# Kernel optimization log

Measured on AMD Instinct MI355X. Metric: run time of the kernel, lower is better.

Reference implementation:

```python
import jax, jax.numpy as jnp
import numpy as np

K = 5              # kernel_size per pseudo dim
K3 = K ** 3        # 125 kernel weight slots
BITS = np.array([[(c >> d) & 1 for d in range(3)] for c in range(8)], dtype=np.int32)  # [8,3]
STRIDES = np.array([1, K, K * K], dtype=np.int32)

N0, E0 = 16384, 262144
N1, E1 = 4096, 65536
N2, E2 = 1024, 16384
N3, E3 = 256, 4096
B = 16
V = B * 8          # final dense 2x2x2 voxels per graph


def spline_conv(x, src, dst, pseudo, W, root, bias, num_nodes):
    """Degree-1 open B-spline conv (torch SplineConv, mean aggr + root + bias).
    x: [N,in], pseudo: [E,3] in [0,1], W: [K^3,in,out]."""
    v = pseudo * (K - 1)                         # [E,3]
    lo = jnp.clip(jnp.floor(v), 0, K - 2)
    frac = v - lo                                # [E,3]
    lo = lo.astype(jnp.int32)
    bits = jnp.asarray(BITS)                     # [8,3]
    idx = lo[:, None, :] + bits[None]            # [E,8,3]
    kidx = (idx * jnp.asarray(STRIDES)).sum(-1)  # [E,8] flat kernel index
    basis = jnp.where(bits[None].astype(bool), frac[:, None, :], 1.0 - frac[:, None, :]).prod(-1)  # [E,8]
    y = jnp.einsum('ni,kio->nko', x, W)          # [N,K3,out] per-node per-kernel transform
    yv = y[src[:, None], kidx]                   # [E,8,out] gather
    msg = (basis[..., None] * yv).sum(1)         # [E,out]
    agg = jax.ops.segment_sum(msg, dst, num_segments=num_nodes)
    deg = jax.ops.segment_sum(jnp.ones(dst.shape[0], x.dtype), dst, num_segments=num_nodes)
    agg = agg / jnp.maximum(deg, 1.0)[:, None]   # mean aggregation
    return agg + x @ root + bias


def pool_max(x, cluster, num_segments):
    p = jax.ops.segment_max(x, cluster, num_segments=num_segments)
    return jnp.where(jnp.isfinite(p), p, 0.0)    # empty voxels -> 0


def setup_inputs() -> dict:
    key = jax.random.key(0)
    ks = iter(jax.random.split(key, 64))
    f = lambda s, sc: jax.random.normal(next(ks), s, jnp.float32) * sc
    u = lambda s: jax.random.uniform(next(ks), s, jnp.float32)
    ri = lambda s, hi: jax.random.randint(next(ks), s, 0, hi, dtype=jnp.int32)
    return dict(
        x0=u((N0, 1)),
        pseudo0=u((E0, 3)), pseudo1=u((E1, 3)), pseudo2=u((E2, 3)), pseudo3=u((E3, 3)),
        W1=f((K3, 1, 32), 0.3), root1=f((1, 32), 0.3), b1=f((32,), 0.05),
        W2=f((K3, 32, 64), 0.05), root2=f((32, 64), 0.05), b2=f((64,), 0.05),
        W3=f((K3, 64, 64), 0.04), root3=f((64, 64), 0.04), b3=f((64,), 0.05),
        W4=f((K3, 64, 128), 0.04), root4=f((64, 128), 0.04), b4=f((128,), 0.05),
        fc1_w=f((1024, 256), 0.03), fc1_b=f((256,), 0.05),
        fc2_w=f((256, 10), 0.06), fc2_b=f((10,), 0.05),
        src0=ri((E0,), N0), dst0=ri((E0,), N0),
        src1=ri((E1,), N1), dst1=ri((E1,), N1),
        src2=ri((E2,), N2), dst2=ri((E2,), N2),
        src3=ri((E3,), N3), dst3=ri((E3,), N3),
        cluster0=ri((N0,), N1), cluster1=ri((N1,), N2),
        cluster2=ri((N2,), N3), cluster3=ri((N3,), V),
    )


def reference(x0, pseudo0, pseudo1, pseudo2, pseudo3,
              W1, root1, b1, W2, root2, b2, W3, root3, b3, W4, root4, b4,
              fc1_w, fc1_b, fc2_w, fc2_b,
              src0, dst0, src1, dst1, src2, dst2, src3, dst3,
              cluster0, cluster1, cluster2, cluster3):
    x = jax.nn.elu(spline_conv(x0, src0, dst0, pseudo0, W1, root1, b1, N0))
    x = pool_max(x, cluster0, N1)
    x = jax.nn.elu(spline_conv(x, src1, dst1, pseudo1, W2, root2, b2, N1))
    x = pool_max(x, cluster1, N2)
    x = jax.nn.elu(spline_conv(x, src2, dst2, pseudo2, W3, root3, b3, N2))
    x = pool_max(x, cluster2, N3)
    x = jax.nn.elu(spline_conv(x, src3, dst3, pseudo3, W4, root4, b4, N3))
    x = pool_max(x, cluster3, V)                 # [B*8, 128]
    x = x.reshape(B, 8 * 128)
    x = jax.nn.elu(x @ fc1_w + fc1_b)
    x = x @ fc2_w + fc2_b                        # dropout is a no-op in eval
    return jax.nn.log_softmax(x, axis=1)
```

## Files before the change

### kernel.cpp

```cpp
#include <hip/hip_runtime.h>
#include <hip/hip_bf16.h>
#include <math.h>

namespace {

typedef unsigned long long u64;
typedef __attribute__((ext_vector_type(8))) short bf16x8;
typedef __attribute__((ext_vector_type(4))) float f32x4;
typedef __attribute__((ext_vector_type(4))) unsigned uint4e;

constexpr int KK = 5;
constexpr int K3 = 125;
constexpr int N0 = 16384, E0 = 262144;
constexpr int N1 = 4096,  E1 = 65536;
constexpr int N2 = 1024,  E2 = 16384;
constexpr int N3 = 256,   E3 = 4096;
constexpr int E_TOT = E0 + E1 + E2 + E3;
constexpr unsigned ENC_NEG_INF = 0x007FFFFFu;
constexpr int KO2 = K3 * 64, KO3 = K3 * 64, KO4 = K3 * 128;

constexpr size_t A_PENC1 = 0;
constexpr size_t A_PENC2 = A_PENC1 + (size_t)N1 * 32;
constexpr size_t A_PENC3 = A_PENC2 + (size_t)N2 * 64;
constexpr size_t A_PENC4 = A_PENC3 + (size_t)N3 * 64;
constexpr size_t A_PENC_END = A_PENC4 + (size_t)128 * 128;
constexpr size_t PENC_TOTAL = A_PENC_END;

constexpr size_t A_WT2 = A_PENC_END;
constexpr size_t A_WT3 = A_WT2 + (size_t)K3 * 64 * 32 / 2;
constexpr size_t A_WT4 = A_WT3 + (size_t)K3 * 64 * 64 / 2;

constexpr size_t A_OFF0 = A_WT4 + (size_t)K3 * 128 * 64 / 2;
constexpr size_t A_OFF1 = A_OFF0 + (N0 + 4);
constexpr size_t A_OFF2 = A_OFF1 + (N1 + 4);
constexpr size_t A_OFF3 = A_OFF2 + (N2 + 4);
constexpr size_t A_CUR0 = A_OFF3 + (N3 + 4);
constexpr size_t A_CUR1 = A_CUR0 + N0;
constexpr size_t A_CUR2 = A_CUR1 + N1;
constexpr size_t A_CUR3 = A_CUR2 + N2;
constexpr size_t A_CUR_END = A_CUR3 + N3;
constexpr size_t CUR_TOTAL = A_CUR_END - A_CUR0;

constexpr size_t A_REC0 = (A_CUR_END + 3) & ~(size_t)3;
constexpr size_t A_REC1 = A_REC0 + (size_t)E0 * 12;
constexpr size_t A_REC2 = A_REC1 + (size_t)E1 * 12;
constexpr size_t A_REC3 = A_REC2 + (size_t)E2 * 12;
constexpr size_t A_Y    = (A_REC3 + (size_t)E3 * 12 + 3) & ~(size_t)3;

constexpr int NB_HIST  = (E_TOT + 255) / 256;
constexpr int NB_SCAT0 = E0 / 256;
constexpr int NB_SCAT1 = E1 / 256;
constexpr int NB_SCAT2 = E2 / 256;
constexpr int NB_SCAT3 = E3 / 256;
constexpr int NB_L1    = N0 / 8;
constexpr int NB_G2    = (KO2 / 64) * ((N1 / 16) / 16);
constexpr int NB_G3    = (KO3 / 64) * ((N2 / 16) / 16);
constexpr int NB_G4    = (KO4 / 64) * ((N3 / 16) / 16);
constexpr int NB_GA2   = N1 / 4;
constexpr int NB_GA3   = N2 / 4;
constexpr int NB_GA4   = N3 / 4;

struct __align__(16) ERec {
    float4 q0;
    float4 q1;
    u64 kid;
    unsigned src;
    unsigned pad;
};

struct P {
    const float *x0, *W1, *root1, *b1, *root2, *b2, *root3, *b3, *root4, *b4;
    const float *ps0, *ps1, *ps2, *ps3;
    const float *W2, *W3, *W4, *fc1w, *fc1b, *fc2w, *fc2b;
    const int *src0, *dst0, *src1, *dst1, *src2, *dst2, *src3, *dst3;
    const int *cl0, *cl1, *cl2, *cl3;
    float* ws;
    float* out;
};

__device__ __forceinline__ float eluf(float x) { return x > 0.f ? x : expm1f(x); }

__device__ __forceinline__ unsigned enc_f(float x) {
    unsigned u = __float_as_uint(x);
    return (u & 0x80000000u) ? ~u : (u | 0x80000000u);
}
__device__ __forceinline__ float dec_fin(unsigned u) {
    u = (u & 0x80000000u) ? (u & 0x7fffffffu) : ~u;
    float v = __uint_as_float(u);
    return isfinite(v) ? v : 0.f;
}
__device__ __forceinline__ float bf2f(unsigned short u) {
    return __uint_as_float((unsigned)u << 16);
}
__device__ __forceinline__ unsigned short f2bf(float v) {
    __hip_bfloat16 h = __float2bfloat16(v);
    return *reinterpret_cast<unsigned short*>(&h);
}

__device__ __forceinline__ ERec nt_load_rec(const ERec* p) {
    const uint4e* q = (const uint4e*)p;
    uint4e a = __builtin_nontemporal_load(q);
    uint4e b = __builtin_nontemporal_load(q + 1);
    uint4e c = __builtin_nontemporal_load(q + 2);
    ERec r;
    r.q0 = make_float4(__uint_as_float(a[0]), __uint_as_float(a[1]),
                       __uint_as_float(a[2]), __uint_as_float(a[3]));
    r.q1 = make_float4(__uint_as_float(b[0]), __uint_as_float(b[1]),
                       __uint_as_float(b[2]), __uint_as_float(b[3]));
    r.kid = (u64)c[0] | ((u64)c[1] << 32);
    r.src = c[2];
    r.pad = c[3];
    return r;
}
__device__ __forceinline__ void nt_store_rec(ERec* p, const ERec& r) {
    uint4e a = {__float_as_uint(r.q0.x), __float_as_uint(r.q0.y),
                __float_as_uint(r.q0.z), __float_as_uint(r.q0.w)};
    uint4e b = {__float_as_uint(r.q1.x), __float_as_uint(r.q1.y),
                __float_as_uint(r.q1.z), __float_as_uint(r.q1.w)};
    uint4e c = {(unsigned)(r.kid & 0xffffffffu), (unsigned)(r.kid >> 32), r.src, r.pad};
    uint4e* q = (uint4e*)p;
    __builtin_nontemporal_store(a, q);
    __builtin_nontemporal_store(b, q + 1);
    __builtin_nontemporal_store(c, q + 2);
}
__device__ __forceinline__ unsigned short nt_lds(const unsigned short* p) {
    return __builtin_nontemporal_load(p);
}

__device__ __forceinline__ void decode_edge(const float* __restrict__ pseudo, int e,
                                            float bas[8], int kid[8]) {
    float v0 = pseudo[e * 3 + 0] * (KK - 1);
    float v1 = pseudo[e * 3 + 1] * (KK - 1);
    float v2 = pseudo[e * 3 + 2] * (KK - 1);
    float f0 = fminf(fmaxf(floorf(v0), 0.f), (float)(KK - 2));
    float f1 = fminf(fmaxf(floorf(v1), 0.f), (float)(KK - 2));
    float f2 = fminf(fmaxf(floorf(v2), 0.f), (float)(KK - 2));
    int lo0 = (int)f0, lo1 = (int)f1, lo2 = (int)f2;
    float fr0 = v0 - f0, fr1 = v1 - f1, fr2 = v2 - f2;
#pragma unroll
    for (int c = 0; c < 8; ++c) {
        int b0 = c & 1, b1 = (c >> 1) & 1, b2 = (c >> 2) & 1;
        kid[c] = (lo0 + b0) + (lo1 + b1) * KK + (lo2 + b2) * KK * KK;
        bas[c] = (b0 ? fr0 : 1.f - fr0) * (b1 ? fr1 : 1.f - fr1) * (b2 ? fr2 : 1.f - fr2);
    }
}

__device__ void wt_unit(const float* __restrict__ W, unsigned short* __restrict__ wt,
                        int IN, int OUT, int k, float* smem) {
    const float* Wk = W + (size_t)k * IN * OUT;
    unsigned short* wk = wt + (size_t)k * IN * OUT;
    int halves = IN / 32;
    for (int h = 0; h < halves; ++h) {
        __syncthreads();
        for (int idx = threadIdx.x; idx < 32 * OUT; idx += 256) {
            int i = idx / OUT, o = idx % OUT;
            smem[i * (OUT + 1) + o] = Wk[(size_t)(h * 32 + i) * OUT + o];
        }
        __syncthreads();
        for (int idx = threadIdx.x; idx < OUT * 32; idx += 256) {
            int o = idx / 32, i = idx % 32;
            wk[(size_t)o * IN + h * 32 + i] = f2bf(smem[i * (OUT + 1) + o]);
        }
    }
}

__device__ void scat_unit(int u, const float* __restrict__ ps,
                          const int* __restrict__ dst, const int* __restrict__ srcA,
                          int* __restrict__ cur, ERec* __restrict__ rec, int E) {
    int e = u * 256 + threadIdx.x;
    if (e >= E) return;
    float b[8]; int k[8];
    decode_edge(ps, e, b, k);
    u64 pk = 0;
#pragma unroll
    for (int c = 0; c < 8; ++c) pk |= (u64)(unsigned)k[c] << (8 * c);
    int q = atomicAdd(&cur[dst[e]], 1);
    ERec r;
    r.q0 = make_float4(b[0], b[1], b[2], b[3]);
    r.q1 = make_float4(b[4], b[5], b[6], b[7]);
    r.kid = pk;
    r.src = (unsigned)srcA[e];
    r.pad = 0;
    nt_store_rec(&rec[q], r);
}

template <int IN>
__device__ __forceinline__ void gemm_tile(int n0, int ko0,
                                          const unsigned* __restrict__ penc,
                                          const unsigned short* __restrict__ wt,
                                          unsigned short* __restrict__ y, int KO) {
    int lane = threadIdx.x & 63;
    int l15 = lane & 15;
    int kk = (lane >> 4) << 3;
    int rbase = (lane >> 4) << 2;
    f32x4 acc[4];
#pragma unroll
    for (int t = 0; t < 4; ++t) acc[t] = (f32x4){0.f, 0.f, 0.f, 0.f};
#pragma unroll
    for (int s = 0; s < IN / 32; ++s) {
        const unsigned* pp = penc + (size_t)(n0 + l15) * IN + s * 32 + kk;
        uint4 u0 = *(const uint4*)pp;
        uint4 u1 = *(const uint4*)(pp + 4);
        unsigned uu[8] = {u0.x, u0.y, u0.z, u0.w, u1.x, u1.y, u1.z, u1.w};
        bf16x8 bfrag;
#pragma unroll
        for (int t = 0; t < 8; ++t) bfrag[t] = (short)f2bf(dec_fin(uu[t]));
#pragma unroll
        for (int t = 0; t < 4; ++t) {
            bf16x8 afrag = *(const bf16x8*)(wt + (size_t)(ko0 + t * 16 + l15) * IN + s * 32 + kk);
            acc[t] = __builtin_amdgcn_mfma_f32_16x16x32_bf16(afrag, bfrag, acc[t], 0, 0, 0);
        }
    }
#pragma unroll
    for (int t = 0; t < 4; ++t) {
        u64 pk = (u64)f2bf(acc[t][0]) | ((u64)f2bf(acc[t][1]) << 16)
               | ((u64)f2bf(acc[t][2]) << 32) | ((u64)f2bf(acc[t][3]) << 48);
        __builtin_nontemporal_store(pk, (u64*)(y + (size_t)(n0 + l15) * KO + ko0 + t * 16 + rbase));
    }
}

template <int IN>
__device__ void gemm_blk(int bid, const unsigned* __restrict__ penc,
                         const unsigned short* __restrict__ wt,
                         unsigned short* __restrict__ y, int N, int KO) {
    int nGrp = (N >> 4) >> 4;
    int kog = bid / nGrp;
    int nchunk = bid % nGrp;
    int wsub = threadIdx.x >> 6;
    int ko0 = kog << 6;
#pragma unroll
    for (int it = 0; it < 4; ++it) {
        int ntile = (nchunk << 4) + (it << 2) + wsub;
        gemm_tile<IN>(ntile << 4, ko0, penc, wt, y, KO);
    }
}

template <int IN, int OUT>
__device__ void gather_unit(int u, const unsigned short* __restrict__ y,
                            const ERec* __restrict__ rec, const int* __restrict__ off,
                            const unsigned* __restrict__ penc_prev,
                            const float* __restrict__ root,
                            const float* __restrict__ bias,
                            const int* __restrict__ cl,
                            unsigned* __restrict__ penc) {
    constexpr int KO = K3 * OUT;
    constexpr int WPT = OUT / 64;
    int lane = threadIdx.x & 63;
    int wv = threadIdx.x >> 6;
    int n = u * 4 + wv;
    int s0 = off[n], s1 = off[n + 1];
    float acc0 = 0.f, acc1 = 0.f;
    int j = s0;
    for (; j + 2 <= s1; j += 2) {
        ERec ra = nt_load_rec(&rec[j]), rb = nt_load_rec(&rec[j + 1]);
        const unsigned short* ypa = y + (size_t)ra.src * KO + lane;
        const unsigned short* ypb = y + (size_t)rb.src * KO + lane;
        float ba[8] = {ra.q0.x, ra.q0.y, ra.q0.z, ra.q0.w, ra.q1.x, ra.q1.y, ra.q1.z, ra.q1.w};
        float bb[8] = {rb.q0.x, rb.q0.y, rb.q0.z, rb.q0.w, rb.q1.x, rb.q1.y, rb.q1.z, rb.q1.w};
        u64 ka = ra.kid, kb = rb.kid;
        float va[8], vb[8], va2[8], vb2[8];
#pragma unroll
        for (int c = 0; c < 8; ++c) {
            int kca = (int)((ka >> (8 * c)) & 255u);
            int kcb = (int)((kb >> (8 * c)) & 255u);
            va[c] = bf2f(nt_lds(ypa + (size_t)kca * OUT));
            vb[c] = bf2f(nt_lds(ypb + (size_t)kcb * OUT));
            if (WPT == 2) {
                va2[c] = bf2f(nt_lds(ypa + (size_t)kca * OUT + 64));
                vb2[c] = bf2f(nt_lds(ypb + (size_t)kcb * OUT + 64));
            }
        }
#pragma unroll
        for (int c = 0; c < 8; ++c) {
            acc0 = fmaf(ba[c], va[c], acc0);
            acc0 = fmaf(bb[c], vb[c], acc0);
            if (WPT == 2) {
                acc1 = fmaf(ba[c], va2[c], acc1);
                acc1 = fmaf(bb[c], vb2[c], acc1);
            }
        }
    }
    if (j < s1) {
        ERec r = nt_load_rec(&rec[j]);
        const unsigned short* yp = y + (size_t)r.src * KO + lane;
        float b[8] = {r.q0.x, r.q0.y, r.q0.z, r.q0.w, r.q1.x, r.q1.y, r.q1.z, r.q1.w};
        u64 k8 = r.kid;
#pragma unroll
        for (int c = 0; c < 8; ++c) {
            int kc = (int)((k8 >> (8 * c)) & 255u);
            acc0 = fmaf(b[c], bf2f(nt_lds(yp + (size_t)kc * OUT)), acc0);
            if (WPT == 2) acc1 = fmaf(b[c], bf2f(nt_lds(yp + (size_t)kc * OUT + 64)), acc1);
        }
    }
    float dg = fmaxf((float)(s1 - s0), 1.f);
    float accs[2] = {acc0, acc1};
#pragma unroll
    for (int w = 0; w < WPT; ++w) {
        int o = lane + 64 * w;
        float r = 0.f;
        for (int i = 0; i < IN; ++i)
            r = fmaf(dec_fin(penc_prev[(size_t)n * IN + i]), root[(size_t)i * OUT + o], r);
        float val = accs[w] / dg + r + bias[o];
        val = eluf(val);
        atomicMax(&penc[(size_t)cl[n] * OUT + o], enc_f(val));
    }
}


__global__ __launch_bounds__(256) void k_p1(P p) {
    __shared__ float smem[32 * 129];
    float* ws = p.ws;
    int bid = blockIdx.x;
    if (bid < NB_HIST) {
        int g = bid * 256 + threadIdx.x;
        if (g < (int)PENC_TOTAL) ((unsigned*)(ws + A_PENC1))[g] = ENC_NEG_INF;
        if (g >= E_TOT) return;
        const int* dst; int* cur; int e;
        if (g < E0)                { dst = p.dst0; cur = (int*)(ws + A_CUR0); e = g; }
        else if (g < E0 + E1)      { dst = p.dst1; cur = (int*)(ws + A_CUR1); e = g - E0; }
        else if (g < E0 + E1 + E2) { dst = p.dst2; cur = (int*)(ws + A_CUR2); e = g - E0 - E1; }
        else                       { dst = p.dst3; cur = (int*)(ws + A_CUR3); e = g - E0 - E1 - E2; }
        atomicAdd(&cur[dst[e]], 1);
    } else {
        wt_unit(p.W2, (unsigned short*)(ws + A_WT2), 32, 64, bid - NB_HIST, smem);
    }
}

__global__ __launch_bounds__(1024) void k_scan(P p) {
    __shared__ int ls[1024];
    float* ws = p.ws;
    int* cur; int* off; int N;
    switch (blockIdx.x) {
        case 0:  cur = (int*)(ws + A_CUR0); off = (int*)(ws + A_OFF0); N = N0; break;
        case 1:  cur = (int*)(ws + A_CUR1); off = (int*)(ws + A_OFF1); N = N1; break;
        case 2:  cur = (int*)(ws + A_CUR2); off = (int*)(ws + A_OFF2); N = N2; break;
        default: cur = (int*)(ws + A_CUR3); off = (int*)(ws + A_OFF3); N = N3; break;
    }
    int t = threadIdx.x;
    int chunk = (N + 1023) >> 10;
    int b0 = t * chunk;
    int b1 = min(b0 + chunk, N);
    int s = 0;
    for (int i = b0; i < b1; ++i) s += cur[i];
    ls[t] = s;
    __syncthreads();
    for (int d = 1; d < 1024; d <<= 1) {
        int v = (t >= d) ? ls[t - d] : 0;
        __syncthreads();
        ls[t] += v;
        __syncthreads();
    }
    int run = (t == 0) ? 0 : ls[t - 1];
    for (int i = b0; i < b1; ++i) {
        int c = cur[i];
        off[i] = run;
        cur[i] = run;
        run += c;
    }
    if (t == 1023) off[N] = run;
}

__global__ __launch_bounds__(256) void k_p2(P p) {
    scat_unit(blockIdx.x, p.ps0, p.dst0, p.src0,
              (int*)(p.ws + A_CUR0), (ERec*)(p.ws + A_REC0), E0);
}

__global__ __launch_bounds__(256) void k_l1(P p) {
    __shared__ float wlds[K3 * 32];
    float* ws = p.ws;
    int bid = blockIdx.x;
    if (bid >= NB_L1) {
        scat_unit(bid - NB_L1, p.ps1, p.dst1, p.src1,
                  (int*)(ws + A_CUR1), (ERec*)(ws + A_REC1), E1);
        return;
    }
    for (int i = threadIdx.x; i < K3 * 32; i += 256) wlds[i] = p.W1[i];
    __syncthreads();
    const ERec* rec = (const ERec*)(ws + A_REC0);
    const int* off = (const int*)(ws + A_OFF0);
    unsigned* penc = (unsigned*)(ws + A_PENC1);
    int o = threadIdx.x & 31;
    int nsub = threadIdx.x >> 5;
    int n = bid * 8 + nsub;
    int s0 = off[n], s1 = off[n + 1];
    float acc = 0.f;
    int j = s0;
    for (; j + 2 <= s1; j += 2) {
        ERec ra = nt_load_rec(&rec[j]), rb = nt_load_rec(&rec[j + 1]);
        u64 ka = ra.kid, kb = rb.kid;
        float xa = p.x0[ra.src], xb = p.x0[rb.src];
        float ma, mb;
        ma  = ra.q0.x * wlds[((int)( ka        & 255u)) * 32 + o];
        ma += ra.q0.y * wlds[((int)((ka >>  8) & 255u)) * 32 + o];
        ma += ra.q0.z * wlds[((int)((ka >> 16) & 255u)) * 32 + o];
        ma += ra.q0.w * wlds[((int)((ka >> 24) & 255u)) * 32 + o];
        ma += ra.q1.x * wlds[((int)((ka >> 32) & 255u)) * 32 + o];
        ma += ra.q1.y * wlds[((int)((ka >> 40) & 255u)) * 32 + o];
        ma += ra.q1.z * wlds[((int)((ka >> 48) & 255u)) * 32 + o];
        ma += ra.q1.w * wlds[((int)((ka >> 56) & 255u)) * 32 + o];
        mb  = rb.q0.x * wlds[((int)( kb        & 255u)) * 32 + o];
        mb += rb.q0.y * wlds[((int)((kb >>  8) & 255u)) * 32 + o];
        mb += rb.q0.z * wlds[((int)((kb >> 16) & 255u)) * 32 + o];
        mb += rb.q0.w * wlds[((int)((kb >> 24) & 255u)) * 32 + o];
        mb += rb.q1.x * wlds[((int)((kb >> 32) & 255u)) * 32 + o];
        mb += rb.q1.y * wlds[((int)((kb >> 40) & 255u)) * 32 + o];
        mb += rb.q1.z * wlds[((int)((kb >> 48) & 255u)) * 32 + o];
        mb += rb.q1.w * wlds[((int)((kb >> 56) & 255u)) * 32 + o];
        acc = fmaf(xa, ma, fmaf(xb, mb, acc));
    }
    if (j < s1) {
        ERec r = nt_load_rec(&rec[j]);
        u64 k8 = r.kid;
        float xv = p.x0[r.src];
        float m;
        m  = r.q0.x * wlds[((int)( k8        & 255u)) * 32 + o];
        m += r.q0.y * wlds[((int)((k8 >>  8) & 255u)) * 32 + o];
        m += r.q0.z * wlds[((int)((k8 >> 16) & 255u)) * 32 + o];
        m += r.q0.w * wlds[((int)((k8 >> 24) & 255u)) * 32 + o];
        m += r.q1.x * wlds[((int)((k8 >> 32) & 255u)) * 32 + o];
        m += r.q1.y * wlds[((int)((k8 >> 40) & 255u)) * 32 + o];
        m += r.q1.z * wlds[((int)((k8 >> 48) & 255u)) * 32 + o];
        m += r.q1.w * wlds[((int)((k8 >> 56) & 255u)) * 32 + o];
        acc = fmaf(xv, m, acc);
    }
    float dg = fmaxf((float)(s1 - s0), 1.f);
    float val = acc / dg + p.x0[n] * p.root1[o] + p.b1[o];
    val = eluf(val);
    atomicMax(&penc[(size_t)p.cl0[n] * 32 + o], enc_f(val));
}

__global__ __launch_bounds__(256) void k_g2(P p) {
    __shared__ float smem[32 * 129];
    float* ws = p.ws;
    int bid = blockIdx.x;
    if (bid < NB_G2) {
        gemm_blk<32>(bid, (unsigned*)(ws + A_PENC1), (unsigned short*)(ws + A_WT2),
                     (unsigned short*)(ws + A_Y), N1, KO2);
    } else if (bid < NB_G2 + NB_SCAT2) {
        scat_unit(bid - NB_G2, p.ps2, p.dst2, p.src2,
                  (int*)(ws + A_CUR2), (ERec*)(ws + A_REC2), E2);
    } else if (bid < NB_G2 + NB_SCAT2 + K3) {
        wt_unit(p.W3, (unsigned short*)(ws + A_WT3), 64, 64, bid - NB_G2 - NB_SCAT2, smem);
    } else {
        wt_unit(p.W4, (unsigned short*)(ws + A_WT4), 64, 128, bid - NB_G2 - NB_SCAT2 - K3, smem);
    }
}

__global__ __launch_bounds__(256) void k_ga2(P p) {
    float* ws = p.ws;
    int bid = blockIdx.x;
    if (bid < NB_GA2) {
        gather_unit<32, 64>(bid, (unsigned short*)(ws + A_Y), (const ERec*)(ws + A_REC1),
                            (const int*)(ws + A_OFF1), (unsigned*)(ws + A_PENC1),
                            p.root2, p.b2, p.cl1, (unsigned*)(ws + A_PENC2));
    } else {
        scat_unit(bid - NB_GA2, p.ps3, p.dst3, p.src3,
                  (int*)(ws + A_CUR3), (ERec*)(ws + A_REC3), E3);
    }
}

__global__ __launch_bounds__(256) void k_g3(P p) {
    gemm_blk<64>(blockIdx.x, (unsigned*)(p.ws + A_PENC2), (unsigned short*)(p.ws + A_WT3),
                 (unsigned short*)(p.ws + A_Y), N2, KO3);
}
__global__ __launch_bounds__(256) void k_ga3(P p) {
    gather_unit<64, 64>(blockIdx.x, (unsigned short*)(p.ws + A_Y), (const ERec*)(p.ws + A_REC2),
                        (const int*)(p.ws + A_OFF2), (unsigned*)(p.ws + A_PENC2),
                        p.root3, p.b3, p.cl2, (unsigned*)(p.ws + A_PENC3));
}
__global__ __launch_bounds__(256) void k_g4(P p) {
    gemm_blk<64>(blockIdx.x, (unsigned*)(p.ws + A_PENC3), (unsigned short*)(p.ws + A_WT4),
                 (unsigned short*)(p.ws + A_Y), N3, KO4);
}
__global__ __launch_bounds__(256) void k_ga4(P p) {
    gather_unit<64, 128>(blockIdx.x, (unsigned short*)(p.ws + A_Y), (const ERec*)(p.ws + A_REC3),
                         (const int*)(p.ws + A_OFF3), (unsigned*)(p.ws + A_PENC3),
                         p.root4, p.b4, p.cl3, (unsigned*)(p.ws + A_PENC4));
}

__global__ __launch_bounds__(1024) void k_fc(P p) {
    __shared__ float xs[1024];
    __shared__ float part[4][257];
    __shared__ float h[256];
    __shared__ float l[10];
    __shared__ float red[2];
    int bq = blockIdx.x;
    int t = threadIdx.x;
    const unsigned* penc4 = (const unsigned*)(p.ws + A_PENC4);
    xs[t] = dec_fin(penc4[(size_t)bq * 1024 + t]);
    __syncthreads();
    int o = t & 255, sl = t >> 8;
    const float* wp = p.fc1w + (size_t)(sl * 256) * 256 + o;
    const float* xp = xs + sl * 256;
    float acc = 0.f;
#pragma unroll 8
    for (int k = 0; k < 256; ++k)
        acc = fmaf(xp[k], wp[(size_t)k * 256], acc);
    part[sl][o] = acc;
    __syncthreads();
    if (t < 256) {
        float v = part[0][t] + part[1][t] + part[2][t] + part[3][t] + p.fc1b[t];
        h[t] = eluf(v);
    }
    __syncthreads();
    if (t < 10) {
        float a2 = p.fc2b[t];
        for (int q = 0; q < 256; ++q)
            a2 = fmaf(h[q], p.fc2w[(size_t)q * 10 + t], a2);
        l[t] = a2;
    }
    __syncthreads();
    if (t == 0) {
        float m = l[0];
        for (int i = 1; i < 10; ++i) m = fmaxf(m, l[i]);
        float s = 0.f;
        for (int i = 0; i < 10; ++i) s += expf(l[i] - m);
        red[0] = m;
        red[1] = logf(s);
    }
    __syncthreads();
    if (t < 10) p.out[(size_t)bq * 10 + t] = l[t] - red[0] - red[1];
}

}

extern "C" void kernel_launch(void* const* d_in, const int* in_sizes, int n_in,
                              void* d_out, int out_size, void* d_ws, size_t ws_size,
                              hipStream_t stream) {
    P p;
    p.x0    = (const float*)d_in[0];
    p.ps0   = (const float*)d_in[1];
    p.ps1   = (const float*)d_in[2];
    p.ps2   = (const float*)d_in[3];
    p.ps3   = (const float*)d_in[4];
    p.W1    = (const float*)d_in[5];
    p.root1 = (const float*)d_in[6];
    p.b1    = (const float*)d_in[7];
    p.W2    = (const float*)d_in[8];
    p.root2 = (const float*)d_in[9];
    p.b2    = (const float*)d_in[10];
    p.W3    = (const float*)d_in[11];
    p.root3 = (const float*)d_in[12];
    p.b3    = (const float*)d_in[13];
    p.W4    = (const float*)d_in[14];
    p.root4 = (const float*)d_in[15];
    p.b4    = (const float*)d_in[16];
    p.fc1w  = (const float*)d_in[17];
    p.fc1b  = (const float*)d_in[18];
    p.fc2w  = (const float*)d_in[19];
    p.fc2b  = (const float*)d_in[20];
    p.src0 = (const int*)d_in[21];
    p.dst0 = (const int*)d_in[22];
    p.src1 = (const int*)d_in[23];
    p.dst1 = (const int*)d_in[24];
    p.src2 = (const int*)d_in[25];
    p.dst2 = (const int*)d_in[26];
    p.src3 = (const int*)d_in[27];
    p.dst3 = (const int*)d_in[28];
    p.cl0  = (const int*)d_in[29];
    p.cl1  = (const int*)d_in[30];
    p.cl2  = (const int*)d_in[31];
    p.cl3  = (const int*)d_in[32];
    p.ws = (float*)d_ws;
    p.out = (float*)d_out;

    hipMemsetAsync(p.ws + A_CUR0, 0, CUR_TOTAL * sizeof(int), stream);

    k_p1 <<<NB_HIST + K3, 256, 0, stream>>>(p);
    k_scan<<<4, 1024, 0, stream>>>(p);
    k_p2 <<<NB_SCAT0, 256, 0, stream>>>(p);
    k_l1 <<<NB_L1 + NB_SCAT1, 256, 0, stream>>>(p);
    k_g2 <<<NB_G2 + NB_SCAT2 + 2 * K3, 256, 0, stream>>>(p);
    k_ga2<<<NB_GA2 + NB_SCAT3, 256, 0, stream>>>(p);
    k_g3 <<<NB_G3, 256, 0, stream>>>(p);
    k_ga3<<<NB_GA3, 256, 0, stream>>>(p);
    k_g4 <<<NB_G4, 256, 0, stream>>>(p);
    k_ga4<<<NB_GA4, 256, 0, stream>>>(p);
    k_fc <<<16, 1024, 0, stream>>>(p);
}
```

Baseline: 385.6 us.

## Stage GEMM output tiles through LDS and drop nontemporal loads/stores

The MFMA accumulator tiles are now written to a per-wave LDS staging buffer and then copied to global memory as coalesced 16-byte row stores, replacing the scattered 8-byte nontemporal stores. All nontemporal load/store builtins for edge records and gathered y values become plain accesses, so those reads and writes can be cached. This adds LDS traffic and relies on wave-level implicit ordering between the LDS write and the LDS read, with no barrier between them.

New measurement: 322.8 us. 1.19x faster.

```diff
diff --git a/kernel.cpp b/kernel.cpp
--- a/kernel.cpp
+++ b/kernel.cpp
@@ -7,7 +7,6 @@
 typedef unsigned long long u64;
 typedef __attribute__((ext_vector_type(8))) short bf16x8;
 typedef __attribute__((ext_vector_type(4))) float f32x4;
-typedef __attribute__((ext_vector_type(4))) unsigned uint4e;
 
 constexpr int KK = 5;
 constexpr int K3 = 125;
@@ -60,6 +59,9 @@
 constexpr int NB_GA3   = N2 / 4;
 constexpr int NB_GA4   = N3 / 4;
 
+constexpr int STG_STRIDE = 72;
+constexpr int STG_PER_WAVE = 16 * STG_STRIDE;
+
 struct __align__(16) ERec {
     float4 q0;
     float4 q1;
@@ -95,36 +97,6 @@
 __device__ __forceinline__ unsigned short f2bf(float v) {
     __hip_bfloat16 h = __float2bfloat16(v);
     return *reinterpret_cast<unsigned short*>(&h);
-}
-
-__device__ __forceinline__ ERec nt_load_rec(const ERec* p) {
-    const uint4e* q = (const uint4e*)p;
-    uint4e a = __builtin_nontemporal_load(q);
-    uint4e b = __builtin_nontemporal_load(q + 1);
-    uint4e c = __builtin_nontemporal_load(q + 2);
-    ERec r;
-    r.q0 = make_float4(__uint_as_float(a[0]), __uint_as_float(a[1]),
-                       __uint_as_float(a[2]), __uint_as_float(a[3]));
-    r.q1 = make_float4(__uint_as_float(b[0]), __uint_as_float(b[1]),
-                       __uint_as_float(b[2]), __uint_as_float(b[3]));
-    r.kid = (u64)c[0] | ((u64)c[1] << 32);
-    r.src = c[2];
-    r.pad = c[3];
-    return r;
-}
-__device__ __forceinline__ void nt_store_rec(ERec* p, const ERec& r) {
-    uint4e a = {__float_as_uint(r.q0.x), __float_as_uint(r.q0.y),
-                __float_as_uint(r.q0.z), __float_as_uint(r.q0.w)};
-    uint4e b = {__float_as_uint(r.q1.x), __float_as_uint(r.q1.y),
-                __float_as_uint(r.q1.z), __float_as_uint(r.q1.w)};
-    uint4e c = {(unsigned)(r.kid & 0xffffffffu), (unsigned)(r.kid >> 32), r.src, r.pad};
-    uint4e* q = (uint4e*)p;
-    __builtin_nontemporal_store(a, q);
-    __builtin_nontemporal_store(b, q + 1);
-    __builtin_nontemporal_store(c, q + 2);
-}
-__device__ __forceinline__ unsigned short nt_lds(const unsigned short* p) {
-    return __builtin_nontemporal_load(p);
 }
 
 __device__ __forceinline__ void decode_edge(const float* __restrict__ pseudo, int e,
@@ -181,14 +153,15 @@
     r.kid = pk;
     r.src = (unsigned)srcA[e];
     r.pad = 0;
-    nt_store_rec(&rec[q], r);
+    rec[q] = r;
 }
 
 template <int IN>
 __device__ __forceinline__ void gemm_tile(int n0, int ko0,
                                           const unsigned* __restrict__ penc,
                                           const unsigned short* __restrict__ wt,
-                                          unsigned short* __restrict__ y, int KO) {
+                                          unsigned short* __restrict__ y, int KO,
+                                          unsigned short* __restrict__ stg) {
     int lane = threadIdx.x & 63;
     int l15 = lane & 15;
     int kk = (lane >> 4) << 3;
@@ -213,25 +186,36 @@
     }
 #pragma unroll
     for (int t = 0; t < 4; ++t) {
-        u64 pk = (u64)f2bf(acc[t][0]) | ((u64)f2bf(acc[t][1]) << 16)
-               | ((u64)f2bf(acc[t][2]) << 32) | ((u64)f2bf(acc[t][3]) << 48);
-        __builtin_nontemporal_store(pk, (u64*)(y + (size_t)(n0 + l15) * KO + ko0 + t * 16 + rbase));
+#pragma unroll
+        for (int j = 0; j < 4; ++j)
+            stg[l15 * STG_STRIDE + t * 16 + rbase + j] = f2bf(acc[t][j]);
+    }
+#pragma unroll
+    for (int i = 0; i < 2; ++i) {
+        int idx = i * 64 + lane;
+        int row = idx >> 3;
+        int off8 = (idx & 7) << 3;
+        const uint4* s = (const uint4*)(stg + row * STG_STRIDE + off8);
+        uint4 v = *s;
+        *(uint4*)(y + (size_t)(n0 + row) * KO + ko0 + off8) = v;
     }
 }
 
 template <int IN>
 __device__ void gemm_blk(int bid, const unsigned* __restrict__ penc,
                          const unsigned short* __restrict__ wt,
-                         unsigned short* __restrict__ y, int N, int KO) {
+                         unsigned short* __restrict__ y, int N, int KO,
+                         unsigned short* __restrict__ stg_base) {
     int nGrp = (N >> 4) >> 4;
     int kog = bid / nGrp;
     int nchunk = bid % nGrp;
     int wsub = threadIdx.x >> 6;
     int ko0 = kog << 6;
+    unsigned short* stg = stg_base + wsub * STG_PER_WAVE;
 #pragma unroll
     for (int it = 0; it < 4; ++it) {
         int ntile = (nchunk << 4) + (it << 2) + wsub;
-        gemm_tile<IN>(ntile << 4, ko0, penc, wt, y, KO);
+        gemm_tile<IN>(ntile << 4, ko0, penc, wt, y, KO, stg);
     }
 }
 
@@ -252,7 +236,7 @@
     float acc0 = 0.f, acc1 = 0.f;
     int j = s0;
     for (; j + 2 <= s1; j += 2) {
-        ERec ra = nt_load_rec(&rec[j]), rb = nt_load_rec(&rec[j + 1]);
+        ERec ra = rec[j], rb = rec[j + 1];
         const unsigned short* ypa = y + (size_t)ra.src * KO + lane;
         const unsigned short* ypb = y + (size_t)rb.src * KO + lane;
         float ba[8] = {ra.q0.x, ra.q0.y, ra.q0.z, ra.q0.w, ra.q1.x, ra.q1.y, ra.q1.z, ra.q1.w};
@@ -263,11 +247,11 @@
         for (int c = 0; c < 8; ++c) {
             int kca = (int)((ka >> (8 * c)) & 255u);
             int kcb = (int)((kb >> (8 * c)) & 255u);
-            va[c] = bf2f(nt_lds(ypa + (size_t)kca * OUT));
-            vb[c] = bf2f(nt_lds(ypb + (size_t)kcb * OUT));
+            va[c] = bf2f(ypa[(size_t)kca * OUT]);
+            vb[c] = bf2f(ypb[(size_t)kcb * OUT]);
             if (WPT == 2) {
-                va2[c] = bf2f(nt_lds(ypa + (size_t)kca * OUT + 64));
-                vb2[c] = bf2f(nt_lds(ypb + (size_t)kcb * OUT + 64));
+                va2[c] = bf2f(ypa[(size_t)kca * OUT + 64]);
+                vb2[c] = bf2f(ypb[(size_t)kcb * OUT + 64]);
             }
         }
 #pragma unroll
@@ -281,15 +265,15 @@
         }
     }
     if (j < s1) {
-        ERec r = nt_load_rec(&rec[j]);
+        ERec r = rec[j];
         const unsigned short* yp = y + (size_t)r.src * KO + lane;
         float b[8] = {r.q0.x, r.q0.y, r.q0.z, r.q0.w, r.q1.x, r.q1.y, r.q1.z, r.q1.w};
         u64 k8 = r.kid;
 #pragma unroll
         for (int c = 0; c < 8; ++c) {
             int kc = (int)((k8 >> (8 * c)) & 255u);
-            acc0 = fmaf(b[c], bf2f(nt_lds(yp + (size_t)kc * OUT)), acc0);
-            if (WPT == 2) acc1 = fmaf(b[c], bf2f(nt_lds(yp + (size_t)kc * OUT + 64)), acc1);
+            acc0 = fmaf(b[c], bf2f(yp[(size_t)kc * OUT]), acc0);
+            if (WPT == 2) acc1 = fmaf(b[c], bf2f(yp[(size_t)kc * OUT + 64]), acc1);
         }
     }
     float dg = fmaxf((float)(s1 - s0), 1.f);
@@ -386,7 +370,7 @@
     float acc = 0.f;
     int j = s0;
     for (; j + 2 <= s1; j += 2) {
-        ERec ra = nt_load_rec(&rec[j]), rb = nt_load_rec(&rec[j + 1]);
+        ERec ra = rec[j], rb = rec[j + 1];
         u64 ka = ra.kid, kb = rb.kid;
         float xa = p.x0[ra.src], xb = p.x0[rb.src];
         float ma, mb;
@@ -409,7 +393,7 @@
         acc = fmaf(xa, ma, fmaf(xb, mb, acc));
     }
     if (j < s1) {
-        ERec r = nt_load_rec(&rec[j]);
+        ERec r = rec[j];
         u64 k8 = r.kid;
         float xv = p.x0[r.src];
         float m;
@@ -435,7 +419,7 @@
     int bid = blockIdx.x;
     if (bid < NB_G2) {
         gemm_blk<32>(bid, (unsigned*)(ws + A_PENC1), (unsigned short*)(ws + A_WT2),
-                     (unsigned short*)(ws + A_Y), N1, KO2);
+                     (unsigned short*)(ws + A_Y), N1, KO2, (unsigned short*)smem);
     } else if (bid < NB_G2 + NB_SCAT2) {
         scat_unit(bid - NB_G2, p.ps2, p.dst2, p.src2,
                   (int*)(ws + A_CUR2), (ERec*)(ws + A_REC2), E2);
@@ -460,8 +444,9 @@
 }
 
 __global__ __launch_bounds__(256) void k_g3(P p) {
+    __shared__ unsigned short stg[4 * STG_PER_WAVE];
     gemm_blk<64>(blockIdx.x, (unsigned*)(p.ws + A_PENC2), (unsigned short*)(p.ws + A_WT3),
-                 (unsigned short*)(p.ws + A_Y), N2, KO3);
+                 (unsigned short*)(p.ws + A_Y), N2, KO3, stg);
 }
 __global__ __launch_bounds__(256) void k_ga3(P p) {
     gather_unit<64, 64>(blockIdx.x, (unsigned short*)(p.ws + A_Y), (const ERec*)(p.ws + A_REC2),
@@ -469,8 +454,9 @@
                         p.root3, p.b3, p.cl2, (unsigned*)(p.ws + A_PENC3));
 }
 __global__ __launch_bounds__(256) void k_g4(P p) {
+    __shared__ unsigned short stg[4 * STG_PER_WAVE];
     gemm_blk<64>(blockIdx.x, (unsigned*)(p.ws + A_PENC3), (unsigned short*)(p.ws + A_WT4),
-                 (unsigned short*)(p.ws + A_Y), N3, KO4);
+                 (unsigned short*)(p.ws + A_Y), N3, KO4, stg);
 }
 __global__ __launch_bounds__(256) void k_ga4(P p) {
     gather_unit<64, 128>(blockIdx.x, (unsigned short*)(p.ws + A_Y), (const ERec*)(p.ws + A_REC3),
```
